# Optimization experiments

Hardware: AMD Instinct MI355X
Metric: run time of the kernel (lower is better)

## Reference

```python
import jax, jax.numpy as jnp
import numpy as np

N = 100000      # nodes
E = 1600000     # edges (avg degree 16)
FEAT = 128
EMBED = 64
CLS = 40


def setup_inputs() -> dict:
    key = jax.random.key(0)
    k1, k2, k3, k4 = jax.random.split(key, 4)
    x = jax.random.normal(k1, (N, FEAT), dtype=jnp.float32)
    edge_index = jax.random.randint(k2, (2, E), 0, N, dtype=jnp.int32)
    W1 = jax.random.normal(k3, (FEAT, EMBED), dtype=jnp.float32) / np.sqrt(FEAT).astype(np.float32)
    b1 = jnp.zeros((EMBED,), dtype=jnp.float32)
    W2 = jax.random.normal(k4, (EMBED, CLS), dtype=jnp.float32) / np.sqrt(EMBED).astype(np.float32)
    b2 = jnp.zeros((CLS,), dtype=jnp.float32)
    return {"x": x, "edge_index": edge_index, "W1": W1, "b1": b1, "W2": W2, "b2": b2}


def gcn_conv(x, edge_index, W, b):
    """PyG GCNConv: linear -> add self loops -> symmetric-norm scatter-add -> bias."""
    n = x.shape[0]
    x = x @ W                                   # [n, out_dim]
    loops = jnp.arange(n, dtype=edge_index.dtype)
    row = jnp.concatenate([edge_index[0], loops])  # source nodes
    col = jnp.concatenate([edge_index[1], loops])  # destination nodes
    # degree after self-loops (in-degree over destination index)
    deg = jax.ops.segment_sum(jnp.ones_like(col, dtype=x.dtype), col, num_segments=n)
    dinv = jnp.where(deg > 0, jax.lax.rsqrt(deg), 0.0)
    norm = dinv[row] * dinv[col]                # [E+n]
    msg = x[row] * norm[:, None]                # gather + scale
    out = jax.ops.segment_sum(msg, col, num_segments=n)  # scatter-add
    return out + b


def reference(x, edge_index, W1, b1, W2, b2):
    h = jax.nn.relu(gcn_conv(x, edge_index, W1, b1))
    logits = gcn_conv(h, edge_index, W2, b2)
    return jax.nn.log_softmax(logits, axis=1)
```

## Files before the change

### kernel.cpp

```cpp
#include <hip/hip_runtime.h>
#include <math.h>

#define FEAT 128
#define EMBED 64
#define CLS 40

#define GRP 512
#define GSH 9
#define STRIDE 12288
#define T1 2048

typedef __attribute__((ext_vector_type(8))) short s8v;
typedef __attribute__((ext_vector_type(4))) float f32x4;

static __device__ __forceinline__ float bf2f(unsigned short u) {
    union { unsigned int i; float f; } c; c.i = ((unsigned int)u) << 16; return c.f;
}
static __device__ __forceinline__ unsigned short f2bf(float f) {
    union { float f; unsigned int i; } c; c.f = f;
    unsigned int x = c.i;
    x += 0x7fffu + ((x >> 16) & 1u);
    return (unsigned short)(x >> 16);
}


__global__ void k_initcur(int* __restrict__ cursor, int B) {
    int t = blockIdx.x * blockDim.x + threadIdx.x;
    if (t < B) cursor[t] = t * STRIDE;
}


__global__ __launch_bounds__(256) void k_p1(const int* __restrict__ ei,
                                            unsigned long long* __restrict__ pairs,
                                            int* __restrict__ cursor, int E, int B) {
    __shared__ unsigned long long pl[T1];
    __shared__ int hist[256], base[256], gbase[256], lcnt[256], scanbuf[256];
    int tid = threadIdx.x;
    int tile0 = blockIdx.x * T1;
    int cnt = min(T1, E - tile0);

    hist[tid] = 0; lcnt[tid] = 0;
    __syncthreads();

    int s[T1 / 256], d[T1 / 256];
#pragma unroll
    for (int i = 0; i < T1 / 256; ++i) {
        int k = i * 256 + tid;
        if (k < cnt) {
            s[i] = ei[tile0 + k];
            d[i] = ei[E + tile0 + k];
            atomicAdd(&hist[d[i] >> GSH], 1);
        }
    }
    __syncthreads();

    int h = hist[tid];
    scanbuf[tid] = h;
    __syncthreads();
    for (int off = 1; off < 256; off <<= 1) {
        int t = (tid >= (unsigned)off) ? scanbuf[tid - off] : 0;
        __syncthreads();
        scanbuf[tid] += t;
        __syncthreads();
    }
    base[tid] = scanbuf[tid] - h;
    gbase[tid] = (tid < B && h > 0) ? atomicAdd(&cursor[tid], h) : 0;
    __syncthreads();

#pragma unroll
    for (int i = 0; i < T1 / 256; ++i) {
        int k = i * 256 + tid;
        if (k < cnt) {
            int b = d[i] >> GSH;
            int pos = base[b] + atomicAdd(&lcnt[b], 1);
            pl[pos] = ((unsigned long long)(unsigned)d[i] << 32) | (unsigned)s[i];
        }
    }
    __syncthreads();

    for (int k = tid; k < cnt; k += 256) {
        unsigned long long p = pl[k];
        int b = (int)(p >> (32 + GSH));
        pairs[(size_t)gbase[b] + (k - base[b])] = p;
    }
}


__global__ void k_bscan(const int* __restrict__ cursor, int* __restrict__ csrBase,
                        int* __restrict__ rowptr, int B, int E, int N) {
    __shared__ int sh[256];
    int t = threadIdx.x;
    int c = (t < B) ? cursor[t] - t * STRIDE : 0;
    sh[t] = c;
    __syncthreads();
    for (int off = 1; off < 256; off <<= 1) {
        int u = (t >= off) ? sh[t - off] : 0;
        __syncthreads();
        sh[t] += u;
        __syncthreads();
    }
    if (t < B) csrBase[t] = sh[t] - c;
    if (t == 0) rowptr[N] = E;
}


__global__ __launch_bounds__(512) void k_p2(const unsigned long long* __restrict__ pairs,
                                            const int* __restrict__ cursor,
                                            const int* __restrict__ csrBase,
                                            int* __restrict__ csr, int* __restrict__ rowptr,
                                            float* __restrict__ dinv, int N) {
    __shared__ int hist[GRP], cur[GRP], scanbuf[GRP];
    int t = threadIdx.x;
    int b = blockIdx.x;
    int v0 = b << GSH;
    size_t reg0 = (size_t)b * STRIDE;
    int cnt = cursor[b] - b * STRIDE;

    hist[t] = 0;
    __syncthreads();
    for (int k = t; k < cnt; k += GRP)
        atomicAdd(&hist[(int)(pairs[reg0 + k] >> 32) - v0], 1);
    __syncthreads();

    int h = hist[t];
    scanbuf[t] = h;
    __syncthreads();
    for (int off = 1; off < GRP; off <<= 1) {
        int u = (t >= off) ? scanbuf[t - off] : 0;
        __syncthreads();
        scanbuf[t] += u;
        __syncthreads();
    }
    int excl = scanbuf[t] - h;
    int cB = csrBase[b];
    int v = v0 + t;
    if (v < N) {
        rowptr[v] = cB + excl;
        dinv[v] = rsqrtf((float)(h + 1));
    }
    cur[t] = excl;
    __syncthreads();

    for (int k = t; k < cnt; k += GRP) {
        unsigned long long p = pairs[reg0 + k];
        int l = (int)(p >> 32) - v0;
        int pos = atomicAdd(&cur[l], 1);
        csr[cB + pos] = (int)(p & 0xffffffffu);
    }
}


__global__ __launch_bounds__(256) void k_gemm1(const float* __restrict__ x,
                                               const float* __restrict__ W1,
                                               const float* __restrict__ dinv,
                                               unsigned short* __restrict__ A1, int N) {
    __shared__ unsigned short Wt[EMBED * 136];
    for (int i = threadIdx.x; i < FEAT * EMBED; i += 256) {
        int k = i >> 6, n = i & 63;
        Wt[n * 136 + k] = f2bf(W1[i]);
    }
    __syncthreads();

    int wv = threadIdx.x >> 6, lane = threadIdx.x & 63;
    int g = lane >> 4, r = lane & 15;
    int arow = blockIdx.x * 64 + wv * 16 + r;
    bool rowok = arow < N;
    float dv = rowok ? dinv[arow] : 0.f;

    s8v a[4];
#pragma unroll
    for (int ks = 0; ks < 4; ++ks) {
        if (rowok) {
            const float* p = x + (size_t)arow * FEAT + ks * 32 + g * 8;
            float4 p0 = *(const float4*)p;
            float4 p1 = *(const float4*)(p + 4);
            s8v t;
            t[0] = (short)f2bf(p0.x * dv); t[1] = (short)f2bf(p0.y * dv);
            t[2] = (short)f2bf(p0.z * dv); t[3] = (short)f2bf(p0.w * dv);
            t[4] = (short)f2bf(p1.x * dv); t[5] = (short)f2bf(p1.y * dv);
            t[6] = (short)f2bf(p1.z * dv); t[7] = (short)f2bf(p1.w * dv);
            a[ks] = t;
        } else {
            s8v z = {};
            a[ks] = z;
        }
    }

    f32x4 acc[4];
#pragma unroll
    for (int nt = 0; nt < 4; ++nt) acc[nt] = (f32x4){0.f, 0.f, 0.f, 0.f};

#pragma unroll
    for (int nt = 0; nt < 4; ++nt) {
        int n0 = nt * 16;
#pragma unroll
        for (int ks = 0; ks < 4; ++ks) {
            s8v bfr = *(const s8v*)&Wt[(n0 + r) * 136 + ks * 32 + g * 8];
            acc[nt] = __builtin_amdgcn_mfma_f32_16x16x32_bf16(a[ks], bfr, acc[nt], 0, 0, 0);
        }
    }

    int orow0 = blockIdx.x * 64 + wv * 16 + g * 4;
#pragma unroll
    for (int nt = 0; nt < 4; ++nt)
#pragma unroll
        for (int q = 0; q < 4; ++q) {
            int orow = orow0 + q;
            if (orow < N) A1[(size_t)orow * EMBED + nt * 16 + r] = f2bf(acc[nt][q]);
        }
}


#define ACC8(u)                                                              \
    a0 += bf2f((unsigned short)(u)[0]); a1 += bf2f((unsigned short)(u)[1]);  \
    a2 += bf2f((unsigned short)(u)[2]); a3 += bf2f((unsigned short)(u)[3]);  \
    a4 += bf2f((unsigned short)(u)[4]); a5 += bf2f((unsigned short)(u)[5]);  \
    a6 += bf2f((unsigned short)(u)[6]); a7 += bf2f((unsigned short)(u)[7]);

#define GATHER_ACC(TBL)                                                      \
    float a0=0,a1=0,a2=0,a3=0,a4=0,a5=0,a6=0,a7=0;                           \
    for (int p = rs; p < cnt; p += 32) {                                     \
        int pA = p, pB = p + 8, pC = p + 16, pD = p + 24;                    \
        int sA = (pA < cnt - 1) ? csr[beg + pA] : v;                         \
        int sB = (pB < cnt - 1) ? csr[beg + pB] : v;                         \
        int sC = (pC < cnt - 1) ? csr[beg + pC] : v;                         \
        int sD = (pD < cnt - 1) ? csr[beg + pD] : v;                         \
        { s8v u = *(const s8v*)(TBL + (size_t)sA * EMBED + dp); ACC8(u) }    \
        if (pB < cnt) { s8v u = *(const s8v*)(TBL + (size_t)sB * EMBED + dp); ACC8(u) } \
        if (pC < cnt) { s8v u = *(const s8v*)(TBL + (size_t)sC * EMBED + dp); ACC8(u) } \
        if (pD < cnt) { s8v u = *(const s8v*)(TBL + (size_t)sD * EMBED + dp); ACC8(u) } \
    }                                                                        \
    _Pragma("unroll")                                                        \
    for (int o = 8; o < 64; o <<= 1) {                                       \
        a0 += __shfl_xor(a0, o); a1 += __shfl_xor(a1, o);                    \
        a2 += __shfl_xor(a2, o); a3 += __shfl_xor(a3, o);                    \
        a4 += __shfl_xor(a4, o); a5 += __shfl_xor(a5, o);                    \
        a6 += __shfl_xor(a6, o); a7 += __shfl_xor(a7, o);                    \
    }

__global__ __launch_bounds__(256) void k_gf1(const int* __restrict__ rowptr,
                                             const int* __restrict__ csr,
                                             const unsigned short* __restrict__ A1,
                                             const float* __restrict__ dinv,
                                             const float* __restrict__ b1,
                                             unsigned short* __restrict__ Hb, int N) {
    int wv = threadIdx.x >> 6, lane = threadIdx.x & 63;
    int v = blockIdx.x * 4 + wv;
    if (v >= N) return;
    int beg = rowptr[v];
    int cnt = rowptr[v + 1] - beg + 1;
    int rs = lane >> 3, dp = (lane & 7) * 8;

    GATHER_ACC(A1)

    if (rs == 0) {
        float dv = dinv[v];
        float4 bA = *(const float4*)(b1 + dp);
        float4 bB = *(const float4*)(b1 + dp + 4);
        float h0 = fmaxf(dv * a0 + bA.x, 0.f), h1 = fmaxf(dv * a1 + bA.y, 0.f);
        float h2 = fmaxf(dv * a2 + bA.z, 0.f), h3 = fmaxf(dv * a3 + bA.w, 0.f);
        float h4 = fmaxf(dv * a4 + bB.x, 0.f), h5 = fmaxf(dv * a5 + bB.y, 0.f);
        float h6 = fmaxf(dv * a6 + bB.z, 0.f), h7 = fmaxf(dv * a7 + bB.w, 0.f);
        s8v o;
        o[0] = (short)f2bf(h0 * dv); o[1] = (short)f2bf(h1 * dv);
        o[2] = (short)f2bf(h2 * dv); o[3] = (short)f2bf(h3 * dv);
        o[4] = (short)f2bf(h4 * dv); o[5] = (short)f2bf(h5 * dv);
        o[6] = (short)f2bf(h6 * dv); o[7] = (short)f2bf(h7 * dv);
        *(s8v*)(Hb + (size_t)v * EMBED + dp) = o;
    }
}

__global__ __launch_bounds__(256) void k_gf2h(const int* __restrict__ rowptr,
                                              const int* __restrict__ csr,
                                              const unsigned short* __restrict__ Hb,
                                              const float* __restrict__ dinv,
                                              unsigned short* __restrict__ Pb, int N) {
    int wv = threadIdx.x >> 6, lane = threadIdx.x & 63;
    int v = blockIdx.x * 4 + wv;
    if (v >= N) return;
    int beg = rowptr[v];
    int cnt = rowptr[v + 1] - beg + 1;
    int rs = lane >> 3, dp = (lane & 7) * 8;

    GATHER_ACC(Hb)

    if (rs == 0) {
        float dv = dinv[v];
        s8v o;
        o[0] = (short)f2bf(dv * a0); o[1] = (short)f2bf(dv * a1);
        o[2] = (short)f2bf(dv * a2); o[3] = (short)f2bf(dv * a3);
        o[4] = (short)f2bf(dv * a4); o[5] = (short)f2bf(dv * a5);
        o[6] = (short)f2bf(dv * a6); o[7] = (short)f2bf(dv * a7);
        *(s8v*)(Pb + (size_t)v * EMBED + dp) = o;
    }
}


__global__ __launch_bounds__(256) void k_fin(const unsigned short* __restrict__ Pb,
                                             const float* __restrict__ W2,
                                             const float* __restrict__ b2,
                                             float* __restrict__ out, int N) {
    __shared__ unsigned short Wt[48 * 72];
    for (int i = threadIdx.x; i < 48 * EMBED; i += 256) {
        int n = i >> 6, k = i & 63;
        Wt[n * 72 + k] = (n < CLS) ? f2bf(W2[k * CLS + n]) : 0;
    }
    __syncthreads();

    int wv = threadIdx.x >> 6, lane = threadIdx.x & 63;
    int g = lane >> 4, r = lane & 15;
    int arow = blockIdx.x * 64 + wv * 16 + r;

    s8v z = {};
    s8v a[2];
#pragma unroll
    for (int ks = 0; ks < 2; ++ks)
        a[ks] = (arow < N) ? *(const s8v*)(Pb + (size_t)arow * EMBED + ks * 32 + g * 8) : z;

    f32x4 acc[3];
#pragma unroll
    for (int nt = 0; nt < 3; ++nt) acc[nt] = (f32x4){0.f, 0.f, 0.f, 0.f};

#pragma unroll
    for (int nt = 0; nt < 3; ++nt)
#pragma unroll
        for (int ks = 0; ks < 2; ++ks) {
            s8v bfr = *(const s8v*)&Wt[(nt * 16 + r) * 72 + ks * 32 + g * 8];
            acc[nt] = __builtin_amdgcn_mfma_f32_16x16x32_bf16(a[ks], bfr, acc[nt], 0, 0, 0);
        }

    int orow0 = blockIdx.x * 64 + wv * 16 + g * 4;
    bool v2 = r < (CLS - 32);
#pragma unroll
    for (int q = 0; q < 4; ++q) {
        float l0 = acc[0][q] + b2[r];
        float l1 = acc[1][q] + b2[16 + r];
        float l2 = v2 ? acc[2][q] + b2[32 + r] : -INFINITY;
        float m = fmaxf(fmaxf(l0, l1), l2);
#pragma unroll
        for (int o = 1; o < 16; o <<= 1) m = fmaxf(m, __shfl_xor(m, o));
        float se = __expf(l0 - m) + __expf(l1 - m) + (v2 ? __expf(l2 - m) : 0.f);
#pragma unroll
        for (int o = 1; o < 16; o <<= 1) se += __shfl_xor(se, o);
        float lse = m + __logf(se);
        int orow = orow0 + q;
        if (orow < N) {
            float* op = out + (size_t)orow * CLS;
            op[r] = l0 - lse;
            op[16 + r] = l1 - lse;
            if (v2) op[32 + r] = l2 - lse;
        }
    }
}


extern "C" void kernel_launch(void* const* d_in, const int* in_sizes, int n_in,
                              void* d_out, int out_size, void* d_ws, size_t ws_size,
                              hipStream_t stream) {
    const float* x  = (const float*)d_in[0];
    const int*   ei = (const int*)d_in[1];
    const float* W1 = (const float*)d_in[2];
    const float* b1 = (const float*)d_in[3];
    const float* W2 = (const float*)d_in[4];
    const float* b2 = (const float*)d_in[5];
    float* out = (float*)d_out;

    const int N = in_sizes[0] / FEAT;
    const int E = in_sizes[1] / 2;
    const int B = (N + GRP - 1) >> GSH;

    char* ws = (char*)d_ws;
    size_t off = 0;
    auto alloc = [&](size_t bytes) { char* p = ws + off; off = (off + bytes + 255) & ~(size_t)255; return p; };
    int*   cursor  = (int*)alloc(256 * 4);
    int*   csrBase = (int*)alloc(256 * 4);
    float* dinv    = (float*)alloc((size_t)N * 4);
    int*   rowptr  = (int*)alloc((size_t)(N + 1) * 4);
    int*   csr     = (int*)alloc((size_t)E * 4);
    size_t regA = (size_t)B * STRIDE * 8;
    size_t regB = (size_t)N * EMBED * 4;
    char*  region = alloc(regA > regB ? regA : regB);
    unsigned long long* pairs = (unsigned long long*)region;
    unsigned short* A1 = (unsigned short*)region;
    unsigned short* Hb = (unsigned short*)(region + (size_t)N * EMBED * 2);
    unsigned short* Pb = A1;

    k_initcur<<<1, 256, 0, stream>>>(cursor, B);
    k_p1<<<(E + T1 - 1) / T1, 256, 0, stream>>>(ei, pairs, cursor, E, B);
    k_bscan<<<1, 256, 0, stream>>>(cursor, csrBase, rowptr, B, E, N);
    k_p2<<<B, GRP, 0, stream>>>(pairs, cursor, csrBase, csr, rowptr, dinv, N);

    k_gemm1<<<(N + 63) / 64, 256, 0, stream>>>(x, W1, dinv, A1, N);
    k_gf1<<<(N + 3) / 4, 256, 0, stream>>>(rowptr, csr, A1, dinv, b1, Hb, N);
    k_gf2h<<<(N + 3) / 4, 256, 0, stream>>>(rowptr, csr, Hb, dinv, Pb, N);
    k_fin<<<(N + 63) / 64, 256, 0, stream>>>(Pb, W2, b2, out, N);
}
```

Measured before the change: 164.1 us.

## Process two nodes per wavefront in gather kernels to overlap row loads

Each wavefront in the two neighbour-gather kernels now handles two consecutive destination nodes. It issues all index and row loads for both nodes up front, then accumulates, with a separate tail loop for degrees above 32. The aim is to raise memory-level parallelism and hide gather latency, since the original loop issued loads for one node at a time with dependent index reads. This halves the grid size and raises register pressure. Load balance may also suffer when the two nodes have very different degrees.

Result: faster. 142.3 us (-13.2%).

```diff
diff --git a/kernel.cpp b/kernel.cpp
--- a/kernel.cpp
+++ b/kernel.cpp
@@ -211,32 +211,54 @@
 }
 
 
-#define ACC8(u)                                                              \
-    a0 += bf2f((unsigned short)(u)[0]); a1 += bf2f((unsigned short)(u)[1]);  \
-    a2 += bf2f((unsigned short)(u)[2]); a3 += bf2f((unsigned short)(u)[3]);  \
-    a4 += bf2f((unsigned short)(u)[4]); a5 += bf2f((unsigned short)(u)[5]);  \
-    a6 += bf2f((unsigned short)(u)[6]); a7 += bf2f((unsigned short)(u)[7]);
-
-#define GATHER_ACC(TBL)                                                      \
-    float a0=0,a1=0,a2=0,a3=0,a4=0,a5=0,a6=0,a7=0;                           \
-    for (int p = rs; p < cnt; p += 32) {                                     \
-        int pA = p, pB = p + 8, pC = p + 16, pD = p + 24;                    \
-        int sA = (pA < cnt - 1) ? csr[beg + pA] : v;                         \
-        int sB = (pB < cnt - 1) ? csr[beg + pB] : v;                         \
-        int sC = (pC < cnt - 1) ? csr[beg + pC] : v;                         \
-        int sD = (pD < cnt - 1) ? csr[beg + pD] : v;                         \
-        { s8v u = *(const s8v*)(TBL + (size_t)sA * EMBED + dp); ACC8(u) }    \
-        if (pB < cnt) { s8v u = *(const s8v*)(TBL + (size_t)sB * EMBED + dp); ACC8(u) } \
-        if (pC < cnt) { s8v u = *(const s8v*)(TBL + (size_t)sC * EMBED + dp); ACC8(u) } \
-        if (pD < cnt) { s8v u = *(const s8v*)(TBL + (size_t)sD * EMBED + dp); ACC8(u) } \
-    }                                                                        \
-    _Pragma("unroll")                                                        \
-    for (int o = 8; o < 64; o <<= 1) {                                       \
-        a0 += __shfl_xor(a0, o); a1 += __shfl_xor(a1, o);                    \
-        a2 += __shfl_xor(a2, o); a3 += __shfl_xor(a3, o);                    \
-        a4 += __shfl_xor(a4, o); a5 += __shfl_xor(a5, o);                    \
-        a6 += __shfl_xor(a6, o); a7 += __shfl_xor(a7, o);                    \
-    }
+struct I4 { int s0, s1, s2, s3; };
+struct R4 { s8v u0, u1, u2, u3; };
+
+static __device__ __forceinline__ I4 g_idx(const int* __restrict__ csr,
+                                           int beg, int cnt, int v, int rs) {
+    I4 r;
+    r.s0 = (rs      < cnt - 1) ? csr[beg + rs]      : v;
+    r.s1 = (rs + 8  < cnt - 1) ? csr[beg + rs + 8]  : v;
+    r.s2 = (rs + 16 < cnt - 1) ? csr[beg + rs + 16] : v;
+    r.s3 = (rs + 24 < cnt - 1) ? csr[beg + rs + 24] : v;
+    return r;
+}
+static __device__ __forceinline__ R4 g_rows(const unsigned short* __restrict__ T,
+                                            const I4& i, int dp) {
+    R4 r;
+    r.u0 = *(const s8v*)(T + (size_t)i.s0 * EMBED + dp);
+    r.u1 = *(const s8v*)(T + (size_t)i.s1 * EMBED + dp);
+    r.u2 = *(const s8v*)(T + (size_t)i.s2 * EMBED + dp);
+    r.u3 = *(const s8v*)(T + (size_t)i.s3 * EMBED + dp);
+    return r;
+}
+static __device__ __forceinline__ void accu(float* a, s8v u) {
+#pragma unroll
+    for (int i = 0; i < 8; ++i) a[i] += bf2f((unsigned short)u[i]);
+}
+static __device__ __forceinline__ void g_acc(const R4& r, int rs, int cnt, float* a) {
+    if (rs < cnt)      accu(a, r.u0);
+    if (rs + 8 < cnt)  accu(a, r.u1);
+    if (rs + 16 < cnt) accu(a, r.u2);
+    if (rs + 24 < cnt) accu(a, r.u3);
+}
+static __device__ __forceinline__ void g_tail(const unsigned short* __restrict__ T,
+                                              const int* __restrict__ csr,
+                                              int beg, int cnt, int v, int rs, int dp,
+                                              float* a) {
+    for (int p = 32 + rs; p < cnt; p += 8) {
+        int s = (p < cnt - 1) ? csr[beg + p] : v;
+        s8v u = *(const s8v*)(T + (size_t)s * EMBED + dp);
+        accu(a, u);
+    }
+}
+static __device__ __forceinline__ void fold8(float* a) {
+#pragma unroll
+    for (int o = 8; o < 64; o <<= 1) {
+#pragma unroll
+        for (int i = 0; i < 8; ++i) a[i] += __shfl_xor(a[i], o);
+    }
+}
 
 __global__ __launch_bounds__(256) void k_gf1(const int* __restrict__ rowptr,
                                              const int* __restrict__ csr,
@@ -245,28 +267,61 @@
                                              const float* __restrict__ b1,
                                              unsigned short* __restrict__ Hb, int N) {
     int wv = threadIdx.x >> 6, lane = threadIdx.x & 63;
-    int v = blockIdx.x * 4 + wv;
-    if (v >= N) return;
-    int beg = rowptr[v];
-    int cnt = rowptr[v + 1] - beg + 1;
+    int va = (blockIdx.x * 4 + wv) * 2;
+    if (va >= N) return;
+    int vb = va + 1;
+    bool okB = vb < N;
+    int vB = okB ? vb : va;
     int rs = lane >> 3, dp = (lane & 7) * 8;
 
-    GATHER_ACC(A1)
+    int2 rp01 = *(const int2*)(rowptr + va);
+    int rp2 = okB ? rowptr[vb + 1] : rp01.y;
+    float dvA = dinv[va];
+    float dvB = okB ? dinv[vb] : 0.f;
+    float4 bL = *(const float4*)(b1 + dp);
+    float4 bH = *(const float4*)(b1 + dp + 4);
+
+    int begA = rp01.x, cntA = rp01.y - rp01.x + 1;
+    int begB = rp01.y, cntB = okB ? (rp2 - rp01.y + 1) : 0;
+
+    I4 iA = g_idx(csr, begA, cntA, va, rs);
+    I4 iB = g_idx(csr, begB, cntB, vB, rs);
+    R4 rA = g_rows(A1, iA, dp);
+    R4 rB = g_rows(A1, iB, dp);
+
+    float aA[8] = {0,0,0,0,0,0,0,0}, aB[8] = {0,0,0,0,0,0,0,0};
+    g_acc(rA, rs, cntA, aA);
+    g_acc(rB, rs, cntB, aB);
+    if (cntA > 32) g_tail(A1, csr, begA, cntA, va, rs, dp, aA);
+    if (cntB > 32) g_tail(A1, csr, begB, cntB, vB, rs, dp, aB);
+
+    fold8(aA);
+    fold8(aB);
 
     if (rs == 0) {
-        float dv = dinv[v];
-        float4 bA = *(const float4*)(b1 + dp);
-        float4 bB = *(const float4*)(b1 + dp + 4);
-        float h0 = fmaxf(dv * a0 + bA.x, 0.f), h1 = fmaxf(dv * a1 + bA.y, 0.f);
-        float h2 = fmaxf(dv * a2 + bA.z, 0.f), h3 = fmaxf(dv * a3 + bA.w, 0.f);
-        float h4 = fmaxf(dv * a4 + bB.x, 0.f), h5 = fmaxf(dv * a5 + bB.y, 0.f);
-        float h6 = fmaxf(dv * a6 + bB.z, 0.f), h7 = fmaxf(dv * a7 + bB.w, 0.f);
         s8v o;
-        o[0] = (short)f2bf(h0 * dv); o[1] = (short)f2bf(h1 * dv);
-        o[2] = (short)f2bf(h2 * dv); o[3] = (short)f2bf(h3 * dv);
-        o[4] = (short)f2bf(h4 * dv); o[5] = (short)f2bf(h5 * dv);
-        o[6] = (short)f2bf(h6 * dv); o[7] = (short)f2bf(h7 * dv);
-        *(s8v*)(Hb + (size_t)v * EMBED + dp) = o;
+        float h;
+        h = fmaxf(dvA * aA[0] + bL.x, 0.f); o[0] = (short)f2bf(h * dvA);
+        h = fmaxf(dvA * aA[1] + bL.y, 0.f); o[1] = (short)f2bf(h * dvA);
+        h = fmaxf(dvA * aA[2] + bL.z, 0.f); o[2] = (short)f2bf(h * dvA);
+        h = fmaxf(dvA * aA[3] + bL.w, 0.f); o[3] = (short)f2bf(h * dvA);
+        h = fmaxf(dvA * aA[4] + bH.x, 0.f); o[4] = (short)f2bf(h * dvA);
+        h = fmaxf(dvA * aA[5] + bH.y, 0.f); o[5] = (short)f2bf(h * dvA);
+        h = fmaxf(dvA * aA[6] + bH.z, 0.f); o[6] = (short)f2bf(h * dvA);
+        h = fmaxf(dvA * aA[7] + bH.w, 0.f); o[7] = (short)f2bf(h * dvA);
+        *(s8v*)(Hb + (size_t)va * EMBED + dp) = o;
+        if (okB) {
+            s8v p;
+            h = fmaxf(dvB * aB[0] + bL.x, 0.f); p[0] = (short)f2bf(h * dvB);
+            h = fmaxf(dvB * aB[1] + bL.y, 0.f); p[1] = (short)f2bf(h * dvB);
+            h = fmaxf(dvB * aB[2] + bL.z, 0.f); p[2] = (short)f2bf(h * dvB);
+            h = fmaxf(dvB * aB[3] + bL.w, 0.f); p[3] = (short)f2bf(h * dvB);
+            h = fmaxf(dvB * aB[4] + bH.x, 0.f); p[4] = (short)f2bf(h * dvB);
+            h = fmaxf(dvB * aB[5] + bH.y, 0.f); p[5] = (short)f2bf(h * dvB);
+            h = fmaxf(dvB * aB[6] + bH.z, 0.f); p[6] = (short)f2bf(h * dvB);
+            h = fmaxf(dvB * aB[7] + bH.w, 0.f); p[7] = (short)f2bf(h * dvB);
+            *(s8v*)(Hb + (size_t)vb * EMBED + dp) = p;
+        }
     }
 }
 
@@ -276,22 +331,46 @@
                                               const float* __restrict__ dinv,
                                               unsigned short* __restrict__ Pb, int N) {
     int wv = threadIdx.x >> 6, lane = threadIdx.x & 63;
-    int v = blockIdx.x * 4 + wv;
-    if (v >= N) return;
-    int beg = rowptr[v];
-    int cnt = rowptr[v + 1] - beg + 1;
+    int va = (blockIdx.x * 4 + wv) * 2;
+    if (va >= N) return;
+    int vb = va + 1;
+    bool okB = vb < N;
+    int vB = okB ? vb : va;
     int rs = lane >> 3, dp = (lane & 7) * 8;
 
-    GATHER_ACC(Hb)
+    int2 rp01 = *(const int2*)(rowptr + va);
+    int rp2 = okB ? rowptr[vb + 1] : rp01.y;
+    float dvA = dinv[va];
+    float dvB = okB ? dinv[vb] : 0.f;
+
+    int begA = rp01.x, cntA = rp01.y - rp01.x + 1;
+    int begB = rp01.y, cntB = okB ? (rp2 - rp01.y + 1) : 0;
+
+    I4 iA = g_idx(csr, begA, cntA, va, rs);
+    I4 iB = g_idx(csr, begB, cntB, vB, rs);
+    R4 rA = g_rows(Hb, iA, dp);
+    R4 rB = g_rows(Hb, iB, dp);
+
+    float aA[8] = {0,0,0,0,0,0,0,0}, aB[8] = {0,0,0,0,0,0,0,0};
+    g_acc(rA, rs, cntA, aA);
+    g_acc(rB, rs, cntB, aB);
+    if (cntA > 32) g_tail(Hb, csr, begA, cntA, va, rs, dp, aA);
+    if (cntB > 32) g_tail(Hb, csr, begB, cntB, vB, rs, dp, aB);
+
+    fold8(aA);
+    fold8(aB);
 
     if (rs == 0) {
-        float dv = dinv[v];
         s8v o;
-        o[0] = (short)f2bf(dv * a0); o[1] = (short)f2bf(dv * a1);
-        o[2] = (short)f2bf(dv * a2); o[3] = (short)f2bf(dv * a3);
-        o[4] = (short)f2bf(dv * a4); o[5] = (short)f2bf(dv * a5);
-        o[6] = (short)f2bf(dv * a6); o[7] = (short)f2bf(dv * a7);
-        *(s8v*)(Pb + (size_t)v * EMBED + dp) = o;
+#pragma unroll
+        for (int i = 0; i < 8; ++i) o[i] = (short)f2bf(dvA * aA[i]);
+        *(s8v*)(Pb + (size_t)va * EMBED + dp) = o;
+        if (okB) {
+            s8v p;
+#pragma unroll
+            for (int i = 0; i < 8; ++i) p[i] = (short)f2bf(dvB * aB[i]);
+            *(s8v*)(Pb + (size_t)vb * EMBED + dp) = p;
+        }
     }
 }
 
@@ -391,7 +470,7 @@
     k_p2<<<B, GRP, 0, stream>>>(pairs, cursor, csrBase, csr, rowptr, dinv, N);
 
     k_gemm1<<<(N + 63) / 64, 256, 0, stream>>>(x, W1, dinv, A1, N);
-    k_gf1<<<(N + 3) / 4, 256, 0, stream>>>(rowptr, csr, A1, dinv, b1, Hb, N);
-    k_gf2h<<<(N + 3) / 4, 256, 0, stream>>>(rowptr, csr, Hb, dinv, Pb, N);
+    k_gf1<<<(N + 7) / 8, 256, 0, stream>>>(rowptr, csr, A1, dinv, b1, Hb, N);
+    k_gf2h<<<(N + 7) / 8, 256, 0, stream>>>(rowptr, csr, Hb, dinv, Pb, N);
     k_fin<<<(N + 63) / 64, 256, 0, stream>>>(Pb, W2, b2, out, N);
 }
```
